# Performance work log

Hardware: AMD Instinct MI355X
Metric: run time of the kernel (lower is better)

Reference implementation:

```python
import jax, jax.numpy as jnp
import numpy as np

B, S, D, H = 4, 2048, 1024, 16
HD = D // H
SCALE = HD ** -0.5


def setup_inputs() -> dict:
    key = jax.random.key(0)
    ks = jax.random.split(key, 5)
    std = D ** -0.5
    return {
        "x": jax.random.normal(ks[0], (B, S, D), jnp.float32),
        "wq": jax.random.normal(ks[1], (D, D), jnp.float32) * std,
        "bq": jnp.zeros((D,), jnp.float32),
        "wk": jax.random.normal(ks[2], (D, D), jnp.float32) * std,
        "bk": jnp.zeros((D,), jnp.float32),
        "wv": jax.random.normal(ks[3], (D, D), jnp.float32) * std,
        "bv": jnp.zeros((D,), jnp.float32),
        "wo": jax.random.normal(ks[4], (D, D), jnp.float32) * std,
        "bo": jnp.zeros((D,), jnp.float32),
    }


def reference(x, wq, bq, wk, bk, wv, bv, wo, bo):
    # projections; weights stored as [in, out] so y = x @ w + b
    q = (x @ wq + bq).reshape(B, S, H, HD).transpose(0, 2, 1, 3)  # [B,H,S,HD]
    k = (x @ wk + bk).reshape(B, S, H, HD).transpose(0, 2, 1, 3)
    v = (x @ wv + bv).reshape(B, S, H, HD).transpose(0, 2, 1, 3)
    attn = jnp.einsum("bhqd,bhkd->bhqk", q, k) * SCALE  # [B,H,S,S]
    attn = jax.nn.softmax(attn, axis=-1)
    out = jnp.einsum("bhqk,bhkd->bhqd", attn, v)  # [B,H,S,HD]
    out = out.transpose(0, 2, 1, 3).reshape(B, S, D)
    return out @ wo + bo
```

## Files before the change

### kernel.cpp

```cpp
#include <hip/hip_runtime.h>
#include <stdint.h>


typedef __attribute__((ext_vector_type(8))) short bf16x8;
typedef __attribute__((ext_vector_type(4))) short bf16x4;
typedef __attribute__((ext_vector_type(4))) float f32x4;
typedef unsigned short u16;
typedef unsigned int u32;

#define AS1 __attribute__((address_space(1)))
#define AS3 __attribute__((address_space(3)))

#define SCALE_L2E 0.18033688011112042f

__device__ __forceinline__ void gld_lds16(const void* g, void* l) {
  __builtin_amdgcn_global_load_lds((const AS1 void*)g, (AS3 void*)l, 16, 0, 0);
}

__device__ __forceinline__ u16 f2bf(float f) {
  u32 x = __builtin_bit_cast(u32, f);
  x += 0x7fff + ((x >> 16) & 1);
  return (u16)(x >> 16);
}

__device__ __forceinline__ u16 f2bf_fast(float a) {
#if __has_builtin(__builtin_amdgcn_cvt_pk_bf16_f32)
  auto v = __builtin_amdgcn_cvt_pk_bf16_f32(a, a);
  return (u16)(__builtin_bit_cast(u32, v) & 0xffffu);
#else
  return f2bf(a);
#endif
}

__device__ __forceinline__ float exp2_fast(float x) {
#if __has_builtin(__builtin_amdgcn_exp2f)
  return __builtin_amdgcn_exp2f(x);
#else
  return exp2f(x);
#endif
}

__global__ __launch_bounds__(256) void convert_x(const float* __restrict__ x,
                                                 u16* __restrict__ xb) {
  int i = (blockIdx.x * 256 + threadIdx.x) * 4;
  float4 v = *(const float4*)(x + i);
  ushort4 o;
  o.x = f2bf(v.x); o.y = f2bf(v.y); o.z = f2bf(v.z); o.w = f2bf(v.w);
  *(ushort4*)(xb + i) = o;
}

__global__ __launch_bounds__(256) void pack_weights(
    const float* __restrict__ wq, const float* __restrict__ wk,
    const float* __restrict__ wv, const float* __restrict__ wo,
    u16* __restrict__ wt_qkv, u16* __restrict__ wt_o) {
  __shared__ float tile[64][65];
  int mat = blockIdx.z;
  const float* src = (mat == 0) ? wq : (mat == 1) ? wk : (mat == 2) ? wv : wo;
  int k0 = blockIdx.y * 64, j0 = blockIdx.x * 64;
  int t = threadIdx.x;
  int lr = t >> 6;
  int lc = t & 63;
#pragma unroll
  for (int it = 0; it < 16; ++it) {
    int r = it * 4 + lr;
    tile[r][lc] = src[(size_t)(k0 + r) * 1024 + j0 + lc];
  }
  __syncthreads();
  u16* dst = (mat == 3) ? wt_o : (wt_qkv + (size_t)mat * 1024 * 1024);
#pragma unroll
  for (int it = 0; it < 16; ++it) {
    int nl = it * 4 + lr;
    float v = tile[lc][nl];
    if (mat == 0) v *= SCALE_L2E;
    dst[(size_t)(j0 + nl) * 1024 + k0 + lc] = f2bf(v);
  }
}

template <int MODE>
__global__ __launch_bounds__(256, 2) void gemm_bt(
    const u16* __restrict__ A, const u16* __restrict__ Bt,
    const float* __restrict__ bias0, const float* __restrict__ bias1,
    const float* __restrict__ bias2,
    void* __restrict__ out0v, void* __restrict__ out1v, void* __restrict__ out2v) {
  __shared__ u16 lA[128 * 32];
  __shared__ u16 lB[128 * 32];
  const int K = 1024;
  int tid = threadIdx.x;
  int wave = tid >> 6, lane = tid & 63;

  int bid = blockIdx.x;
  int m0, n0;
  if constexpr (MODE == 0) {
    int xcd = bid & 7, j = bid >> 3;
    n0 = (xcd * 3 + j % 3) * 128;
    m0 = (j / 3) * 128;
  } else {
    n0 = (bid & 7) * 128;
    m0 = (bid >> 3) * 128;
  }
  int wm = (wave & 1) * 64, wn = (wave >> 1) * 64;

  f32x4 acc[4][4];
#pragma unroll
  for (int i = 0; i < 4; ++i)
#pragma unroll
    for (int j = 0; j < 4; ++j) acc[i][j] = f32x4{0.f, 0.f, 0.f, 0.f};

  int srow = lane >> 2;
  int scol = (lane & 3) * 8;

  for (int k0 = 0; k0 < K; k0 += 32) {
#pragma unroll
    for (int c = 0; c < 2; ++c) {
      int rbase = wave * 32 + c * 16;
      gld_lds16(A + (size_t)(m0 + rbase + srow) * K + k0 + scol, lA + rbase * 32);
      gld_lds16(Bt + (size_t)(n0 + rbase + srow) * K + k0 + scol, lB + rbase * 32);
    }
    __syncthreads();
    bf16x8 af[4], bfr[4];
#pragma unroll
    for (int mt = 0; mt < 4; ++mt)
      af[mt] = *(const bf16x8*)(lA + (wm + mt * 16 + (lane & 15)) * 32 + (lane >> 4) * 8);
#pragma unroll
    for (int nt = 0; nt < 4; ++nt)
      bfr[nt] = *(const bf16x8*)(lB + (wn + nt * 16 + (lane & 15)) * 32 + (lane >> 4) * 8);
#pragma unroll
    for (int mt = 0; mt < 4; ++mt)
#pragma unroll
      for (int nt = 0; nt < 4; ++nt)
        acc[mt][nt] = __builtin_amdgcn_mfma_f32_16x16x32_bf16(af[mt], bfr[nt], acc[mt][nt], 0, 0, 0);
    __syncthreads();
  }

  int rbase0 = m0 + wm + (lane >> 4) * 4;
  int cbase = n0 + wn + (lane & 15);
#pragma unroll
  for (int nt = 0; nt < 4; ++nt) {
    int col = cbase + nt * 16;
    if constexpr (MODE == 0) {
      int mat = col >> 10, j = col & 1023;
      const float* bp = (mat == 0) ? bias0 : (mat == 1) ? bias1 : bias2;
      float bv = bp[j];
      if (mat == 0) bv *= SCALE_L2E;
      int h = j >> 6, hd = j & 63;
      if (mat == 2) {
        u16* base = (u16*)out2v;
#pragma unroll
        for (int mt = 0; mt < 4; ++mt) {
          int row0 = rbase0 + mt * 16;
          int b = row0 >> 11, s = row0 & 2047;
          size_t idx = ((size_t)(b * 16 + h) * 64 + hd) * 2048 + s;
          ushort4 pk;
          pk.x = f2bf_fast(acc[mt][nt][0] + bv);
          pk.y = f2bf_fast(acc[mt][nt][1] + bv);
          pk.z = f2bf_fast(acc[mt][nt][2] + bv);
          pk.w = f2bf_fast(acc[mt][nt][3] + bv);
          *(ushort4*)(base + idx) = pk;
        }
      } else {
        u16* base = (mat == 0) ? (u16*)out0v : (u16*)out1v;
#pragma unroll
        for (int mt = 0; mt < 4; ++mt)
#pragma unroll
          for (int r = 0; r < 4; ++r) {
            int row = rbase0 + mt * 16 + r;
            int b = row >> 11, s = row & 2047;
            size_t idx = ((size_t)(b * 16 + h) * 2048 + s) * 64 + hd;
            base[idx] = f2bf_fast(acc[mt][nt][r] + bv);
          }
      }
    } else {
      float bv = bias0[col];
      float* o = (float*)out0v;
#pragma unroll
      for (int mt = 0; mt < 4; ++mt)
#pragma unroll
        for (int r = 0; r < 4; ++r) {
          int row = rbase0 + mt * 16 + r;
          o[(size_t)row * 1024 + col] = acc[mt][nt][r] + bv;
        }
    }
  }
}

__global__ __launch_bounds__(256, 3) void flash_attn(
    const u16* __restrict__ Q, const u16* __restrict__ Kb,
    const u16* __restrict__ Vt, u16* __restrict__ ctx) {
  __shared__ u16 lK[2][64 * 32];
  __shared__ u16 lV[2][64 * 32];
  __shared__ u16 lP[4][32 * 68];
  int tid = threadIdx.x, wave = tid >> 6, lane = tid & 63;

  int F = blockIdx.x;
  int xcd = F & 7, idx = F >> 3;
  int bh = xcd * 8 + (idx >> 4);
  int q0 = (idx & 15) * 128;
  int b = bh >> 4, h = bh & 15;
  const u16* Qp = Q + (size_t)bh * 2048 * 64;
  const u16* Kp = Kb + (size_t)bh * 2048 * 64;
  const u16* Vp = Vt + (size_t)bh * 64 * 2048;

  int c = lane & 15, g = lane >> 4;

  bf16x8 qf[2][2];
#pragma unroll
  for (int t = 0; t < 2; ++t) {
    const u16* qrow = Qp + (size_t)(q0 + wave * 32 + t * 16 + c) * 64 + g * 8;
    qf[t][0] = *(const bf16x8*)qrow;
    qf[t][1] = *(const bf16x8*)(qrow + 32);
  }

  float lsum[2][4];
  f32x4 o[2][4];
#pragma unroll
  for (int t = 0; t < 2; ++t)
#pragma unroll
    for (int r = 0; r < 4; ++r) lsum[t][r] = 0.f;
#pragma unroll
  for (int t = 0; t < 2; ++t)
#pragma unroll
    for (int dt = 0; dt < 4; ++dt) o[t][dt] = f32x4{0.f, 0.f, 0.f, 0.f};

  int srow = lane >> 2;
  int schunk = (((lane & 3) ^ ((lane >> 3) & 3)) * 8);
  int rsw = (c >> 1) & 3;

  u16* lp = lP[wave];

  for (int s0 = 0; s0 < 2048; s0 += 64) {
    int row = wave * 16 + srow;
#pragma unroll
    for (int kk = 0; kk < 2; ++kk) {
      gld_lds16(Kp + (size_t)(s0 + row) * 64 + kk * 32 + schunk, lK[kk] + wave * 512);
      gld_lds16(Vp + (size_t)row * 2048 + s0 + kk * 32 + schunk, lV[kk] + wave * 512);
    }
    __syncthreads();

    bf16x8 kf[2][4];
#pragma unroll
    for (int kk = 0; kk < 2; ++kk)
#pragma unroll
      for (int nt = 0; nt < 4; ++nt)
        kf[kk][nt] = *(const bf16x8*)(lK[kk] + (nt * 16 + c) * 32 + (g ^ rsw) * 8);

#pragma unroll
    for (int t = 0; t < 2; ++t) {
      f32x4 sa[4];
#pragma unroll
      for (int nt = 0; nt < 4; ++nt) sa[nt] = f32x4{0.f, 0.f, 0.f, 0.f};
#pragma unroll
      for (int kk = 0; kk < 2; ++kk)
#pragma unroll
        for (int nt = 0; nt < 4; ++nt)
          sa[nt] = __builtin_amdgcn_mfma_f32_16x16x32_bf16(qf[t][kk], kf[kk][nt], sa[nt], 0, 0, 0);

#pragma unroll
      for (int nt = 0; nt < 4; ++nt)
#pragma unroll
        for (int r = 0; r < 4; ++r) {
          float p = exp2_fast(sa[nt][r]);
          lsum[t][r] += p;
          lp[(t * 16 + g * 4 + r) * 68 + nt * 16 + c] = f2bf_fast(p);
        }
    }

#pragma unroll
    for (int kk = 0; kk < 2; ++kk) {
      bf16x8 vf[4];
#pragma unroll
      for (int dt = 0; dt < 4; ++dt)
        vf[dt] = *(const bf16x8*)(lV[kk] + (dt * 16 + c) * 32 + (g ^ rsw) * 8);
#pragma unroll
      for (int t = 0; t < 2; ++t) {
        const u16* pb = lp + (t * 16 + c) * 68 + kk * 32 + g * 8;
        bf16x4 p0 = *(const bf16x4*)pb;
        bf16x4 p1 = *(const bf16x4*)(pb + 4);
        bf16x8 pf = __builtin_shufflevector(p0, p1, 0, 1, 2, 3, 4, 5, 6, 7);
#pragma unroll
        for (int dt = 0; dt < 4; ++dt)
          o[t][dt] = __builtin_amdgcn_mfma_f32_16x16x32_bf16(pf, vf[dt], o[t][dt], 0, 0, 0);
      }
    }
    __syncthreads();
  }

#pragma unroll
  for (int t = 0; t < 2; ++t)
#pragma unroll
    for (int r = 0; r < 4; ++r) {
      float rs = lsum[t][r];
      rs += __shfl_xor(rs, 1);
      rs += __shfl_xor(rs, 2);
      rs += __shfl_xor(rs, 4);
      rs += __shfl_xor(rs, 8);
      float inv = 1.0f / fmaxf(rs, 1e-30f);
      int s = q0 + wave * 32 + t * 16 + g * 4 + r;
      size_t rowbase = ((size_t)(b * 2048 + s) * 16 + h) * 64;
#pragma unroll
      for (int dt = 0; dt < 4; ++dt)
        ctx[rowbase + dt * 16 + c] = f2bf_fast(o[t][dt][r] * inv);
    }
}

extern "C" void kernel_launch(void* const* d_in, const int* in_sizes, int n_in,
                              void* d_out, int out_size, void* d_ws, size_t ws_size,
                              hipStream_t stream) {
  const float* x  = (const float*)d_in[0];
  const float* wq = (const float*)d_in[1];
  const float* bq = (const float*)d_in[2];
  const float* wk = (const float*)d_in[3];
  const float* bk = (const float*)d_in[4];
  const float* wv = (const float*)d_in[5];
  const float* bv = (const float*)d_in[6];
  const float* wo = (const float*)d_in[7];
  const float* bo = (const float*)d_in[8];

  u16* ws = (u16*)d_ws;
  u16* xb     = ws;
  u16* wt_qkv = xb + (size_t)8192 * 1024;
  u16* wt_o   = wt_qkv + (size_t)3072 * 1024;
  u16* Qb     = wt_o + (size_t)1024 * 1024;
  u16* Kbuf   = Qb + (size_t)8192 * 1024;
  u16* Vtb    = Kbuf + (size_t)8192 * 1024;
  u16* ctx    = Vtb + (size_t)8192 * 1024;

  convert_x<<<8192, 256, 0, stream>>>(x, xb);
  pack_weights<<<dim3(16, 16, 4), 256, 0, stream>>>(wq, wk, wv, wo, wt_qkv, wt_o);
  gemm_bt<0><<<1536, 256, 0, stream>>>(xb, wt_qkv, bq, bk, bv, Qb, Kbuf, Vtb);
  flash_attn<<<1024, 256, 0, stream>>>(Qb, Kbuf, Vtb, ctx);
  gemm_bt<1><<<512, 256, 0, stream>>>(ctx, wt_o, bo, nullptr, nullptr,
                                      d_out, nullptr, nullptr);
}
```

Measured before the change: 299.4 us.

## Compute transposed S tile so P stays in registers, dropping LDS round-trip

Swaps the MFMA operand order so S^T is computed. Each lane then holds a column of exp'd probabilities that can be packed straight into a bf16x4 B-operand for a 16x16x16 MFMA with V, removing the per-wave LDS buffer for P and its scalar stores and reloads. Row sums now need only two cross-lane shuffles, and the output is written as packed ushort4 stores. The trade is 16x16x16 MFMAs for PV (twice as many instructions as the x32 form) and narrower V reads from LDS.

```diff
diff --git a/kernel.cpp b/kernel.cpp
--- a/kernel.cpp
+++ b/kernel.cpp
@@ -29,6 +29,27 @@
   return (u16)(__builtin_bit_cast(u32, v) & 0xffffu);
 #else
   return f2bf(a);
+#endif
+}
+
+__device__ __forceinline__ bf16x4 pack_bf16x4(float a, float b, float c, float d) {
+#if __has_builtin(__builtin_amdgcn_cvt_pk_bf16_f32)
+  u32 lo = __builtin_bit_cast(u32, __builtin_amdgcn_cvt_pk_bf16_f32(a, b));
+  u32 hi = __builtin_bit_cast(u32, __builtin_amdgcn_cvt_pk_bf16_f32(c, d));
+#else
+  u32 lo = (u32)f2bf(a) | ((u32)f2bf(b) << 16);
+  u32 hi = (u32)f2bf(c) | ((u32)f2bf(d) << 16);
+#endif
+  union { u32 w[2]; bf16x4 v; } u;
+  u.w[0] = lo; u.w[1] = hi;
+  return u.v;
+}
+
+__device__ __forceinline__ f32x4 mfma16(bf16x4 a, bf16x4 b, f32x4 c) {
+#if __has_builtin(__builtin_amdgcn_mfma_f32_16x16x16_bf16)
+  return __builtin_amdgcn_mfma_f32_16x16x16_bf16(a, b, c, 0, 0, 0);
+#else
+  return __builtin_amdgcn_mfma_f32_16x16x16bf16_1k(a, b, c, 0, 0, 0);
 #endif
 }
 
@@ -188,7 +209,6 @@
     const u16* __restrict__ Vt, u16* __restrict__ ctx) {
   __shared__ u16 lK[2][64 * 32];
   __shared__ u16 lV[2][64 * 32];
-  __shared__ u16 lP[4][32 * 68];
   int tid = threadIdx.x, wave = tid >> 6, lane = tid & 63;
 
   int F = blockIdx.x;
@@ -210,12 +230,8 @@
     qf[t][1] = *(const bf16x8*)(qrow + 32);
   }
 
-  float lsum[2][4];
+  float lsum[2] = {0.f, 0.f};
   f32x4 o[2][4];
-#pragma unroll
-  for (int t = 0; t < 2; ++t)
-#pragma unroll
-    for (int r = 0; r < 4; ++r) lsum[t][r] = 0.f;
 #pragma unroll
   for (int t = 0; t < 2; ++t)
 #pragma unroll
@@ -225,8 +241,6 @@
   int schunk = (((lane & 3) ^ ((lane >> 3) & 3)) * 8);
   int rsw = (c >> 1) & 3;
 
-  u16* lp = lP[wave];
-
   for (int s0 = 0; s0 < 2048; s0 += 64) {
     int row = wave * 16 + srow;
 #pragma unroll
@@ -236,70 +250,56 @@
     }
     __syncthreads();
 
-    bf16x8 kf[2][4];
-#pragma unroll
-    for (int kk = 0; kk < 2; ++kk)
-#pragma unroll
-      for (int nt = 0; nt < 4; ++nt)
-        kf[kk][nt] = *(const bf16x8*)(lK[kk] + (nt * 16 + c) * 32 + (g ^ rsw) * 8);
-
-#pragma unroll
-    for (int t = 0; t < 2; ++t) {
-      f32x4 sa[4];
-#pragma unroll
-      for (int nt = 0; nt < 4; ++nt) sa[nt] = f32x4{0.f, 0.f, 0.f, 0.f};
-#pragma unroll
-      for (int kk = 0; kk < 2; ++kk)
-#pragma unroll
-        for (int nt = 0; nt < 4; ++nt)
-          sa[nt] = __builtin_amdgcn_mfma_f32_16x16x32_bf16(qf[t][kk], kf[kk][nt], sa[nt], 0, 0, 0);
-
-#pragma unroll
-      for (int nt = 0; nt < 4; ++nt)
-#pragma unroll
-        for (int r = 0; r < 4; ++r) {
-          float p = exp2_fast(sa[nt][r]);
-          lsum[t][r] += p;
-          lp[(t * 16 + g * 4 + r) * 68 + nt * 16 + c] = f2bf_fast(p);
-        }
-    }
-
-#pragma unroll
-    for (int kk = 0; kk < 2; ++kk) {
-      bf16x8 vf[4];
-#pragma unroll
-      for (int dt = 0; dt < 4; ++dt)
-        vf[dt] = *(const bf16x8*)(lV[kk] + (dt * 16 + c) * 32 + (g ^ rsw) * 8);
+    bf16x4 pf[2][4];
+#pragma unroll
+    for (int st = 0; st < 4; ++st) {
+      bf16x8 kf0 = *(const bf16x8*)(lK[0] + (st * 16 + c) * 32 + (g ^ rsw) * 8);
+      bf16x8 kf1 = *(const bf16x8*)(lK[1] + (st * 16 + c) * 32 + (g ^ rsw) * 8);
 #pragma unroll
       for (int t = 0; t < 2; ++t) {
-        const u16* pb = lp + (t * 16 + c) * 68 + kk * 32 + g * 8;
-        bf16x4 p0 = *(const bf16x4*)pb;
-        bf16x4 p1 = *(const bf16x4*)(pb + 4);
-        bf16x8 pf = __builtin_shufflevector(p0, p1, 0, 1, 2, 3, 4, 5, 6, 7);
-#pragma unroll
-        for (int dt = 0; dt < 4; ++dt)
-          o[t][dt] = __builtin_amdgcn_mfma_f32_16x16x32_bf16(pf, vf[dt], o[t][dt], 0, 0, 0);
+        f32x4 sa = __builtin_amdgcn_mfma_f32_16x16x32_bf16(kf0, qf[t][0],
+                       f32x4{0.f, 0.f, 0.f, 0.f}, 0, 0, 0);
+        sa = __builtin_amdgcn_mfma_f32_16x16x32_bf16(kf1, qf[t][1], sa, 0, 0, 0);
+        float p0 = exp2_fast(sa[0]), p1 = exp2_fast(sa[1]);
+        float p2 = exp2_fast(sa[2]), p3 = exp2_fast(sa[3]);
+        lsum[t] += (p0 + p1) + (p2 + p3);
+        pf[t][st] = pack_bf16x4(p0, p1, p2, p3);
       }
     }
+
+#pragma unroll
+    for (int st = 0; st < 4; ++st) {
+      int kk = st >> 1;
+      int chunk = (((st & 1) * 2 + (g >> 1)) ^ rsw) * 8 + (g & 1) * 4;
+#pragma unroll
+      for (int dt = 0; dt < 4; ++dt) {
+        bf16x4 vf = *(const bf16x4*)(lV[kk] + (dt * 16 + c) * 32 + chunk);
+#pragma unroll
+        for (int t = 0; t < 2; ++t)
+          o[t][dt] = mfma16(vf, pf[t][st], o[t][dt]);
+      }
+    }
     __syncthreads();
   }
 
 #pragma unroll
-  for (int t = 0; t < 2; ++t)
-#pragma unroll
-    for (int r = 0; r < 4; ++r) {
-      float rs = lsum[t][r];
-      rs += __shfl_xor(rs, 1);
-      rs += __shfl_xor(rs, 2);
-      rs += __shfl_xor(rs, 4);
-      rs += __shfl_xor(rs, 8);
-      float inv = 1.0f / fmaxf(rs, 1e-30f);
-      int s = q0 + wave * 32 + t * 16 + g * 4 + r;
-      size_t rowbase = ((size_t)(b * 2048 + s) * 16 + h) * 64;
-#pragma unroll
-      for (int dt = 0; dt < 4; ++dt)
-        ctx[rowbase + dt * 16 + c] = f2bf_fast(o[t][dt][r] * inv);
-    }
+  for (int t = 0; t < 2; ++t) {
+    float rs = lsum[t];
+    rs += __shfl_xor(rs, 16);
+    rs += __shfl_xor(rs, 32);
+    float inv = 1.0f / fmaxf(rs, 1e-30f);
+    int q = q0 + wave * 32 + t * 16 + c;
+    size_t rowbase = ((size_t)(b * 2048 + q) * 16 + h) * 64;
+#pragma unroll
+    for (int dt = 0; dt < 4; ++dt) {
+      ushort4 pk;
+      pk.x = f2bf_fast(o[t][dt][0] * inv);
+      pk.y = f2bf_fast(o[t][dt][1] * inv);
+      pk.z = f2bf_fast(o[t][dt][2] * inv);
+      pk.w = f2bf_fast(o[t][dt][3] * inv);
+      *(ushort4*)(ctx + rowbase + dt * 16 + g * 4) = pk;
+    }
+  }
 }
 
 extern "C" void kernel_launch(void* const* d_in, const int* in_sizes, int n_in,
```

After: 299.2 us. About the same (-0.1%).
